# Kernel tuning notes

Measured on AMD Instinct MI355X. Metric: run time of the kernel, lower is better.

## Reference

```python
import jax, jax.numpy as jnp
import numpy as np

N = 4096
D = 256
H = 8
E = 131072
NEG = -1e30  # stands in for -inf; keeps grads NaN-free


def setup_inputs() -> dict:
    key = jax.random.key(0)
    ks = jax.random.split(key, 8)
    s = 1.0 / np.sqrt(D)
    return {
        "x": jax.random.normal(ks[0], (N, D), dtype=jnp.float32),
        "edge_index": jax.random.randint(ks[1], (2, E), 0, N, dtype=jnp.int32),
        "Wq": jax.random.normal(ks[2], (D, D), dtype=jnp.float32) * s,
        "Wk": jax.random.normal(ks[3], (D, D), dtype=jnp.float32) * s,
        "Wv": jax.random.normal(ks[4], (D, D), dtype=jnp.float32) * s,
        "Wo": jax.random.normal(ks[5], (D, D), dtype=jnp.float32) * s,
        "bo": jnp.zeros((D,), dtype=jnp.float32),
        "gamma": jnp.ones((D,), dtype=jnp.float32),
        "beta": jnp.zeros((D,), dtype=jnp.float32),
    }


def reference(x, edge_index, Wq, Wk, Wv, Wo, bo, gamma, beta):
    n, d_model = x.shape
    d_h = d_model // H
    scale = jnp.sqrt(jnp.float32(d_h))

    # mask: True = blocked. Diagonal and graph edges (dst attends to src) unblocked.
    mask = jnp.ones((n, n), dtype=bool)
    diag = jnp.arange(n)
    mask = mask.at[diag, diag].set(False)
    src, dst = edge_index[0], edge_index[1]
    mask = mask.at[dst, src].set(False)

    # projections: torch Linear computes x @ W.T
    Q = (x @ Wq.T).reshape(n, H, d_h).transpose(1, 0, 2)  # [H, N, d_h]
    K = (x @ Wk.T).reshape(n, H, d_h).transpose(1, 0, 2)
    V = (x @ Wv.T).reshape(n, H, d_h).transpose(1, 0, 2)

    scores = jnp.einsum("hnd,hmd->hnm", Q, K) / scale      # [H, N, N]
    scores = jnp.where(mask[None, :, :], NEG, scores)
    attn = jax.nn.softmax(scores, axis=-1)
    attn = jnp.nan_to_num(attn, nan=0.0)

    out = jnp.einsum("hnm,hmd->hnd", attn, V)              # [H, N, d_h]
    out = out.transpose(1, 0, 2).reshape(n, d_model)
    out = out @ Wo.T + bo

    # LayerNorm(x + out), eps=1e-5
    h = x + out
    mu = jnp.mean(h, axis=-1, keepdims=True)
    var = jnp.var(h, axis=-1, keepdims=True)
    return (h - mu) * jax.lax.rsqrt(var + 1e-5) * gamma + beta
```

## Files before the change

kernel.cpp:

```cpp
#include <hip/hip_runtime.h>

#define D_MODEL 256
#define N_HEADS 8
#define D_HEAD 32
#define MAXN 192

typedef __attribute__((ext_vector_type(8))) short bf16x8;
typedef __attribute__((ext_vector_type(4))) float f32x4;

__device__ __forceinline__ unsigned short f2bf(float f) {
    union { float f; unsigned int u; } v; v.f = f;
    unsigned int r = v.u + 0x7fff + ((v.u >> 16) & 1);
    return (unsigned short)(r >> 16);
}
__device__ __forceinline__ float bf2f(unsigned short u) {
    union { unsigned int u; float f; } v; v.u = ((unsigned int)u) << 16;
    return v.f;
}
__device__ __forceinline__ void pack8(const float* __restrict__ p, short* __restrict__ dst) {
    float4 u0 = *(const float4*)p;
    float4 u1 = *(const float4*)(p + 4);
    ushort4 a, b;
    a.x = f2bf(u0.x); a.y = f2bf(u0.y); a.z = f2bf(u0.z); a.w = f2bf(u0.w);
    b.x = f2bf(u1.x); b.y = f2bf(u1.y); b.z = f2bf(u1.z); b.w = f2bf(u1.w);
    *(ushort4*)dst = a;
    *(ushort4*)(dst + 4) = b;
}

__global__ void set_edges_kernel(const int* __restrict__ ei,
                                 unsigned long long* __restrict__ mask,
                                 int E, int n) {
    int e = blockIdx.x * blockDim.x + threadIdx.x;
    int wpr = n >> 6;
    if (e < n)
        atomicOr(&mask[(size_t)e * wpr + (e >> 6)], 1ULL << (e & 63));
    if (e < E) {
        int src = ei[e];
        int dst = ei[E + e];
        atomicOr(&mask[(size_t)dst * wpr + (src >> 6)], 1ULL << (src & 63));
    }
}

__global__ __launch_bounds__(256) void gemm_qkv_kernel(
        const float* __restrict__ x,
        const float* __restrict__ Wq, const float* __restrict__ Wk,
        const float* __restrict__ Wv,
        unsigned short* __restrict__ Qb, unsigned short* __restrict__ Kb,
        unsigned short* __restrict__ Vb) {
    const float* B = (blockIdx.z == 0) ? Wq : (blockIdx.z == 1) ? Wk : Wv;
    unsigned short* Cb = (blockIdx.z == 0) ? Qb : (blockIdx.z == 1) ? Kb : Vb;
    int bx = blockIdx.x, by = blockIdx.y;

    __shared__ short Alds[128][72];
    __shared__ short Blds[64][72];
    int t = threadIdx.x;
    int wave = t >> 6, lane = t & 63;
    int wr = wave >> 1, wc = wave & 1;
    int lr = t >> 3;
    int lk = (t & 7) << 3;

    const float* Abase = x + ((size_t)(by * 128 + lr)) * D_MODEL + lk;
    const float* Bbase = B + ((size_t)(bx * 64 + lr)) * D_MODEL + lk;

    int fm = lane & 15;
    int fk = (lane >> 4) << 3;

    f32x4 acc[4][2];
#pragma unroll
    for (int r = 0; r < 4; ++r)
#pragma unroll
        for (int c = 0; c < 2; ++c) acc[r][c] = (f32x4){0.f, 0.f, 0.f, 0.f};

    for (int k0 = 0; k0 < D_MODEL; k0 += 64) {
        pack8(Abase + k0,               &Alds[lr][lk]);
        pack8(Abase + 32 * D_MODEL + k0, &Alds[lr + 32][lk]);
        pack8(Abase + 64 * D_MODEL + k0, &Alds[lr + 64][lk]);
        pack8(Abase + 96 * D_MODEL + k0, &Alds[lr + 96][lk]);
        pack8(Bbase + k0,               &Blds[lr][lk]);
        pack8(Bbase + 32 * D_MODEL + k0, &Blds[lr + 32][lk]);
        __syncthreads();
#pragma unroll
        for (int ks = 0; ks < 64; ks += 32) {
            bf16x8 af[4], bf[2];
#pragma unroll
            for (int r = 0; r < 4; ++r)
                af[r] = *(const bf16x8*)&Alds[wr * 64 + r * 16 + fm][ks + fk];
#pragma unroll
            for (int c = 0; c < 2; ++c)
                bf[c] = *(const bf16x8*)&Blds[wc * 32 + c * 16 + fm][ks + fk];
#pragma unroll
            for (int r = 0; r < 4; ++r)
#pragma unroll
                for (int c = 0; c < 2; ++c)
                    acc[r][c] = __builtin_amdgcn_mfma_f32_16x16x32_bf16(
                        af[r], bf[c], acc[r][c], 0, 0, 0);
        }
        __syncthreads();
    }

    int orow0 = by * 128 + wr * 64 + ((lane >> 4) << 2);
    int ocol0 = bx * 64 + wc * 32 + (lane & 15);
#pragma unroll
    for (int r = 0; r < 4; ++r)
#pragma unroll
        for (int c = 0; c < 2; ++c)
#pragma unroll
            for (int q = 0; q < 4; ++q)
                Cb[(size_t)(orow0 + r * 16 + q) * D_MODEL + ocol0 + c * 16] =
                    f2bf(acc[r][c][q]);
}

__global__ __launch_bounds__(64) void attn_kernel(
        const unsigned short* __restrict__ Qb, const unsigned short* __restrict__ Kb,
        const unsigned short* __restrict__ Vb,
        const unsigned long long* __restrict__ mask,
        unsigned short* __restrict__ Ob, int n) {
    int dst = blockIdx.x;
    int L = threadIdx.x;
    int wpr = n >> 6;

    __shared__ int nbr[MAXN + 16];
    __shared__ float s_lds[N_HEADS][MAXN];

    unsigned long long w = (L < wpr) ? mask[(size_t)dst * wpr + L] : 0ULL;
    int c = __popcll(w);
    int xs = c;
#pragma unroll
    for (int o = 1; o < 64; o <<= 1) {
        int y = __shfl_up(xs, o, 64);
        if (L >= o) xs += y;
    }
    int pos = xs - c;
    while (w) {
        int b = __builtin_ctzll(w);
        w &= w - 1;
        if (pos < MAXN) nbr[pos] = (L << 6) + b;
        ++pos;
    }
    int cnt = __shfl(xs, 63, 64);
    if (cnt > MAXN) cnt = MAXN;
    int nb = (cnt + 15) & ~15;
    __syncthreads();
    int last = nbr[cnt - 1];
    if (L < nb - cnt) nbr[cnt + L] = last;
    __syncthreads();

    int col = L & 15;
    int kq = L >> 4;
    bf16x8 qf = (bf16x8){0, 0, 0, 0, 0, 0, 0, 0};
    if (col < N_HEADS)
        qf = *(const bf16x8*)(Qb + (size_t)dst * D_MODEL + col * D_HEAD + kq * 8);
    const bf16x8 zf = (bf16x8){0, 0, 0, 0, 0, 0, 0, 0};
    const float inv_scale = 0.17677669529663687f;

    for (int b0 = 0; b0 < nb; b0 += 16) {
        int nj = nbr[b0 + col];
        const unsigned short* krow = Kb + (size_t)nj * D_MODEL + kq * 8;
        f32x4 c0 = (f32x4){0.f, 0.f, 0.f, 0.f};
        f32x4 c1 = (f32x4){0.f, 0.f, 0.f, 0.f};
#pragma unroll
        for (int kb = 0; kb < 8; kb += 2) {
            bf16x8 a0 = *(const bf16x8*)(krow + kb * 32);
            bf16x8 a1 = *(const bf16x8*)(krow + kb * 32 + 32);
            bf16x8 bop0 = (col == kb)     ? qf : zf;
            bf16x8 bop1 = (col == kb + 1) ? qf : zf;
            c0 = __builtin_amdgcn_mfma_f32_16x16x32_bf16(a0, bop0, c0, 0, 0, 0);
            c1 = __builtin_amdgcn_mfma_f32_16x16x32_bf16(a1, bop1, c1, 0, 0, 0);
        }
        if (col < N_HEADS) {
            int jr = b0 + kq * 4;
            float4 o;
            float s0 = (c0[0] + c1[0]) * inv_scale;
            float s1 = (c0[1] + c1[1]) * inv_scale;
            float s2 = (c0[2] + c1[2]) * inv_scale;
            float s3 = (c0[3] + c1[3]) * inv_scale;
            o.x = (jr + 0 < cnt) ? s0 : -1e30f;
            o.y = (jr + 1 < cnt) ? s1 : -1e30f;
            o.z = (jr + 2 < cnt) ? s2 : -1e30f;
            o.w = (jr + 3 < cnt) ? s3 : -1e30f;
            *(float4*)&s_lds[col][jr] = o;
        }
    }
    __syncthreads();

    int h = L >> 3, i = L & 7;
    float m = -1e30f;
    for (int j0 = i * 4; j0 < nb; j0 += 32) {
        float4 v = *(const float4*)&s_lds[h][j0];
        m = fmaxf(m, fmaxf(fmaxf(v.x, v.y), fmaxf(v.z, v.w)));
    }
    m = fmaxf(m, __shfl_xor(m, 1, 8));
    m = fmaxf(m, __shfl_xor(m, 2, 8));
    m = fmaxf(m, __shfl_xor(m, 4, 8));
    float l = 0.f;
    for (int j0 = i * 4; j0 < nb; j0 += 32) {
        float4 v = *(const float4*)&s_lds[h][j0];
        float4 e;
        e.x = __expf(v.x - m); e.y = __expf(v.y - m);
        e.z = __expf(v.z - m); e.w = __expf(v.w - m);
        *(float4*)&s_lds[h][j0] = e;
        l += (e.x + e.y) + (e.z + e.w);
    }
    l += __shfl_xor(l, 1, 8);
    l += __shfl_xor(l, 2, 8);
    l += __shfl_xor(l, 4, 8);
    __syncthreads();

    f32x4 acc = (f32x4){0.f, 0.f, 0.f, 0.f};
    const unsigned short* vb = Vb + 4 * L;
    for (int j = 0; j < nb; j += 4) {
        float4 wv = *(const float4*)&s_lds[h][j];
        int j0 = nbr[j], j1 = nbr[j + 1], j2 = nbr[j + 2], j3 = nbr[j + 3];
        uint2 r0 = *(const uint2*)(vb + (size_t)j0 * D_MODEL);
        uint2 r1 = *(const uint2*)(vb + (size_t)j1 * D_MODEL);
        uint2 r2 = *(const uint2*)(vb + (size_t)j2 * D_MODEL);
        uint2 r3 = *(const uint2*)(vb + (size_t)j3 * D_MODEL);
        acc[0] += wv.x * bf2f((unsigned short)(r0.x & 0xffff));
        acc[1] += wv.x * bf2f((unsigned short)(r0.x >> 16));
        acc[2] += wv.x * bf2f((unsigned short)(r0.y & 0xffff));
        acc[3] += wv.x * bf2f((unsigned short)(r0.y >> 16));
        acc[0] += wv.y * bf2f((unsigned short)(r1.x & 0xffff));
        acc[1] += wv.y * bf2f((unsigned short)(r1.x >> 16));
        acc[2] += wv.y * bf2f((unsigned short)(r1.y & 0xffff));
        acc[3] += wv.y * bf2f((unsigned short)(r1.y >> 16));
        acc[0] += wv.z * bf2f((unsigned short)(r2.x & 0xffff));
        acc[1] += wv.z * bf2f((unsigned short)(r2.x >> 16));
        acc[2] += wv.z * bf2f((unsigned short)(r2.y & 0xffff));
        acc[3] += wv.z * bf2f((unsigned short)(r2.y >> 16));
        acc[0] += wv.w * bf2f((unsigned short)(r3.x & 0xffff));
        acc[1] += wv.w * bf2f((unsigned short)(r3.x >> 16));
        acc[2] += wv.w * bf2f((unsigned short)(r3.y & 0xffff));
        acc[3] += wv.w * bf2f((unsigned short)(r3.y >> 16));
    }
    float rl = 1.f / l;
    ushort4 o;
    o.x = f2bf(acc[0] * rl); o.y = f2bf(acc[1] * rl);
    o.z = f2bf(acc[2] * rl); o.w = f2bf(acc[3] * rl);
    *(ushort4*)(Ob + (size_t)dst * D_MODEL + 4 * L) = o;
}

struct SMemO {
    union {
        struct { short A[64][72]; short B[256][72]; } st;
        float c[64][260];
    };
};

__global__ __launch_bounds__(256) void gemm_o_ln_kernel(
        const unsigned short* __restrict__ Ob, const float* __restrict__ Wo,
        const float* __restrict__ x, const float* __restrict__ bo,
        const float* __restrict__ gamma, const float* __restrict__ beta,
        float* __restrict__ out) {
    __shared__ SMemO sm;
    int by = blockIdx.x;
    int t = threadIdx.x;
    int wave = t >> 6, lane = t & 63;
    int lr = t >> 3;
    int lk = (t & 7) << 3;

    const unsigned short* Abase = Ob + ((size_t)(by * 64 + lr)) * D_MODEL + lk;
    int fm = lane & 15;
    int fk = (lane >> 4) << 3;

    f32x4 acc[16];
#pragma unroll
    for (int ct = 0; ct < 16; ++ct) acc[ct] = (f32x4){0.f, 0.f, 0.f, 0.f};

    for (int k0 = 0; k0 < D_MODEL; k0 += 64) {
        *(uint4*)&sm.st.A[lr][lk]      = *(const uint4*)(Abase + k0);
        *(uint4*)&sm.st.A[lr + 32][lk] = *(const uint4*)(Abase + 32 * D_MODEL + k0);
#pragma unroll
        for (int j = 0; j < 8; ++j)
            pack8(Wo + ((size_t)(lr + 32 * j)) * D_MODEL + k0 + lk,
                  &sm.st.B[lr + 32 * j][lk]);
        __syncthreads();
#pragma unroll
        for (int ks = 0; ks < 64; ks += 32) {
            bf16x8 af = *(const bf16x8*)&sm.st.A[wave * 16 + fm][ks + fk];
#pragma unroll
            for (int ct = 0; ct < 16; ++ct) {
                bf16x8 bf = *(const bf16x8*)&sm.st.B[ct * 16 + fm][ks + fk];
                acc[ct] = __builtin_amdgcn_mfma_f32_16x16x32_bf16(af, bf, acc[ct], 0, 0, 0);
            }
        }
        __syncthreads();
    }

    int rr0 = wave * 16 + ((lane >> 4) << 2);
#pragma unroll
    for (int ct = 0; ct < 16; ++ct)
#pragma unroll
        for (int q = 0; q < 4; ++q)
            sm.c[rr0 + q][ct * 16 + (lane & 15)] = acc[ct][q];
    __syncthreads();

    float4 bo4 = *(const float4*)(bo + lane * 4);
    float4 g4  = *(const float4*)(gamma + lane * 4);
    float4 be4 = *(const float4*)(beta + lane * 4);
    for (int rr = 0; rr < 16; ++rr) {
        int r = wave * 16 + rr;
        int grow = by * 64 + r;
        float4 p = *(const float4*)&sm.c[r][lane * 4];
        float4 xv = *(const float4*)(x + (size_t)grow * D_MODEL + lane * 4);
        float hx = p.x + xv.x + bo4.x;
        float hy = p.y + xv.y + bo4.y;
        float hz = p.z + xv.z + bo4.z;
        float hw = p.w + xv.w + bo4.w;
        float s  = (hx + hy) + (hz + hw);
        float s2 = (hx * hx + hy * hy) + (hz * hz + hw * hw);
#pragma unroll
        for (int o = 32; o; o >>= 1) {
            s  += __shfl_xor(s, o, 64);
            s2 += __shfl_xor(s2, o, 64);
        }
        float mu = s * (1.f / 256.f);
        float var = s2 * (1.f / 256.f) - mu * mu;
        float rstd = rsqrtf(var + 1e-5f);
        float4 o4;
        o4.x = (hx - mu) * rstd * g4.x + be4.x;
        o4.y = (hy - mu) * rstd * g4.y + be4.y;
        o4.z = (hz - mu) * rstd * g4.z + be4.z;
        o4.w = (hw - mu) * rstd * g4.w + be4.w;
        *(float4*)(out + (size_t)grow * D_MODEL + lane * 4) = o4;
    }
}

extern "C" void kernel_launch(void* const* d_in, const int* in_sizes, int n_in,
                              void* d_out, int out_size, void* d_ws, size_t ws_size,
                              hipStream_t stream) {
    const float* x     = (const float*)d_in[0];
    const int*   ei    = (const int*)  d_in[1];
    const float* Wq    = (const float*)d_in[2];
    const float* Wk    = (const float*)d_in[3];
    const float* Wv    = (const float*)d_in[4];
    const float* Wo    = (const float*)d_in[5];
    const float* bo    = (const float*)d_in[6];
    const float* gamma = (const float*)d_in[7];
    const float* beta  = (const float*)d_in[8];
    float* out = (float*)d_out;

    int n = in_sizes[0] / D_MODEL;
    int E = in_sizes[1] / 2;

    char* ws = (char*)d_ws;
    size_t off = 0;
    unsigned long long* mask = (unsigned long long*)(ws + off);
    size_t mask_bytes = (size_t)n * (n >> 6) * sizeof(unsigned long long);
    off += mask_bytes;
    unsigned short* Qb = (unsigned short*)(ws + off); off += (size_t)n * D_MODEL * 2;
    unsigned short* Kb = (unsigned short*)(ws + off); off += (size_t)n * D_MODEL * 2;
    unsigned short* Vb = (unsigned short*)(ws + off); off += (size_t)n * D_MODEL * 2;
    unsigned short* Ob = (unsigned short*)(ws + off); off += (size_t)n * D_MODEL * 2;

    hipMemsetAsync(mask, 0, mask_bytes, stream);
    set_edges_kernel<<<(E + 255) / 256, 256, 0, stream>>>(ei, mask, E, n);

    dim3 gq(D_MODEL / 64, n / 128, 3);
    gemm_qkv_kernel<<<gq, 256, 0, stream>>>(x, Wq, Wk, Wv, Qb, Kb, Vb);

    attn_kernel<<<n, 64, 0, stream>>>(Qb, Kb, Vb, mask, Ob, n);

    gemm_o_ln_kernel<<<n / 64, 256, 0, stream>>>(Ob, Wo, x, bo, gamma, beta, out);
}
```

Baseline: 134.9 us.

## Pre-convert inputs to bf16, fuse mask init with casts and edges with QKV GEMM

A new prep kernel initialises the diagonal mask (replacing the memset) and converts x and all four weight matrices to bf16 once. The QKV GEMM and the edge-scatter atomics now run in one launch on disjoint blocks, and both GEMMs load bf16 tiles directly instead of converting fp32 per tile. The output-projection + LayerNorm kernel halves its row tile to 32 rows so it launches twice as many blocks. This cuts launch count and redundant conversion work, at the cost of extra workspace traffic for the bf16 copies. The prep kernel hardcodes N=4096 and D=256.

```diff
diff --git a/kernel.cpp b/kernel.cpp
--- a/kernel.cpp
+++ b/kernel.cpp
@@ -17,39 +17,70 @@
     union { unsigned int u; float f; } v; v.u = ((unsigned int)u) << 16;
     return v.f;
 }
-__device__ __forceinline__ void pack8(const float* __restrict__ p, short* __restrict__ dst) {
-    float4 u0 = *(const float4*)p;
-    float4 u1 = *(const float4*)(p + 4);
-    ushort4 a, b;
-    a.x = f2bf(u0.x); a.y = f2bf(u0.y); a.z = f2bf(u0.z); a.w = f2bf(u0.w);
-    b.x = f2bf(u1.x); b.y = f2bf(u1.y); b.z = f2bf(u1.z); b.w = f2bf(u1.w);
-    *(ushort4*)dst = a;
-    *(ushort4*)(dst + 4) = b;
-}
-
-__global__ void set_edges_kernel(const int* __restrict__ ei,
-                                 unsigned long long* __restrict__ mask,
-                                 int E, int n) {
-    int e = blockIdx.x * blockDim.x + threadIdx.x;
+
+__global__ void prep_kernel(const float* __restrict__ x,
+                            const float* __restrict__ W0, const float* __restrict__ W1,
+                            const float* __restrict__ W2, const float* __restrict__ W3,
+                            unsigned short* __restrict__ xb,
+                            unsigned short* __restrict__ O0, unsigned short* __restrict__ O1,
+                            unsigned short* __restrict__ O2, unsigned short* __restrict__ O3,
+                            unsigned long long* __restrict__ mask, int n) {
+    const int XV = (4096 * 256) / 4;
+    int i = blockIdx.x * blockDim.x + threadIdx.x;
+
     int wpr = n >> 6;
-    if (e < n)
-        atomicOr(&mask[(size_t)e * wpr + (e >> 6)], 1ULL << (e & 63));
-    if (e < E) {
-        int src = ei[e];
-        int dst = ei[E + e];
-        atomicOr(&mask[(size_t)dst * wpr + (src >> 6)], 1ULL << (src & 63));
-    }
-}
-
-__global__ __launch_bounds__(256) void gemm_qkv_kernel(
-        const float* __restrict__ x,
-        const float* __restrict__ Wq, const float* __restrict__ Wk,
-        const float* __restrict__ Wv,
+    int mwords = n * wpr;
+    if (i < mwords) {
+        int row = i >> 6;
+        int w = i & 63;
+        mask[i] = (w == (row >> 6)) ? (1ULL << (row & 63)) : 0ULL;
+    }
+
+    const float* src;
+    unsigned short* dst;
+    int k;
+    if (i < XV) {
+        src = x; dst = xb; k = i;
+    } else {
+        int i2 = i - XV;
+        if (i2 >= 4 * 16384) return;
+        int z = i2 >> 14;
+        k = i2 & 16383;
+        src = (z == 0) ? W0 : (z == 1) ? W1 : (z == 2) ? W2 : W3;
+        dst = (z == 0) ? O0 : (z == 1) ? O1 : (z == 2) ? O2 : O3;
+    }
+    float4 v = *(const float4*)(src + (size_t)k * 4);
+    ushort4 o;
+    o.x = f2bf(v.x); o.y = f2bf(v.y); o.z = f2bf(v.z); o.w = f2bf(v.w);
+    *(ushort4*)(dst + (size_t)k * 4) = o;
+}
+
+#define NGEMM 384
+
+__global__ __launch_bounds__(256) void qkv_edges_kernel(
+        const unsigned short* __restrict__ xb,
+        const unsigned short* __restrict__ Wq, const unsigned short* __restrict__ Wk,
+        const unsigned short* __restrict__ Wv,
         unsigned short* __restrict__ Qb, unsigned short* __restrict__ Kb,
-        unsigned short* __restrict__ Vb) {
-    const float* B = (blockIdx.z == 0) ? Wq : (blockIdx.z == 1) ? Wk : Wv;
-    unsigned short* Cb = (blockIdx.z == 0) ? Qb : (blockIdx.z == 1) ? Kb : Vb;
-    int bx = blockIdx.x, by = blockIdx.y;
+        unsigned short* __restrict__ Vb,
+        const int* __restrict__ ei, unsigned long long* __restrict__ mask,
+        int E, int n) {
+    int blk = blockIdx.x;
+    if (blk >= NGEMM) {
+        int e = (blk - NGEMM) * 256 + threadIdx.x;
+        if (e < E) {
+            int src = ei[e];
+            int dst = ei[E + e];
+            int wpr = n >> 6;
+            atomicOr(&mask[(size_t)dst * wpr + (src >> 6)], 1ULL << (src & 63));
+        }
+        return;
+    }
+    int z = blk >> 7;
+    int r = blk & 127;
+    int by = r >> 2, bx = r & 3;
+    const unsigned short* B = (z == 0) ? Wq : (z == 1) ? Wk : Wv;
+    unsigned short* Cb = (z == 0) ? Qb : (z == 1) ? Kb : Vb;
 
     __shared__ short Alds[128][72];
     __shared__ short Blds[64][72];
@@ -59,41 +90,41 @@
     int lr = t >> 3;
     int lk = (t & 7) << 3;
 
-    const float* Abase = x + ((size_t)(by * 128 + lr)) * D_MODEL + lk;
-    const float* Bbase = B + ((size_t)(bx * 64 + lr)) * D_MODEL + lk;
+    const unsigned short* Abase = xb + ((size_t)(by * 128 + lr)) * D_MODEL + lk;
+    const unsigned short* Bbase = B + ((size_t)(bx * 64 + lr)) * D_MODEL + lk;
 
     int fm = lane & 15;
     int fk = (lane >> 4) << 3;
 
     f32x4 acc[4][2];
 #pragma unroll
-    for (int r = 0; r < 4; ++r)
-#pragma unroll
-        for (int c = 0; c < 2; ++c) acc[r][c] = (f32x4){0.f, 0.f, 0.f, 0.f};
+    for (int rr = 0; rr < 4; ++rr)
+#pragma unroll
+        for (int c = 0; c < 2; ++c) acc[rr][c] = (f32x4){0.f, 0.f, 0.f, 0.f};
 
     for (int k0 = 0; k0 < D_MODEL; k0 += 64) {
-        pack8(Abase + k0,               &Alds[lr][lk]);
-        pack8(Abase + 32 * D_MODEL + k0, &Alds[lr + 32][lk]);
-        pack8(Abase + 64 * D_MODEL + k0, &Alds[lr + 64][lk]);
-        pack8(Abase + 96 * D_MODEL + k0, &Alds[lr + 96][lk]);
-        pack8(Bbase + k0,               &Blds[lr][lk]);
-        pack8(Bbase + 32 * D_MODEL + k0, &Blds[lr + 32][lk]);
+        *(uint4*)&Alds[lr][lk]      = *(const uint4*)(Abase + k0);
+        *(uint4*)&Alds[lr + 32][lk] = *(const uint4*)(Abase + 32 * D_MODEL + k0);
+        *(uint4*)&Alds[lr + 64][lk] = *(const uint4*)(Abase + 64 * D_MODEL + k0);
+        *(uint4*)&Alds[lr + 96][lk] = *(const uint4*)(Abase + 96 * D_MODEL + k0);
+        *(uint4*)&Blds[lr][lk]      = *(const uint4*)(Bbase + k0);
+        *(uint4*)&Blds[lr + 32][lk] = *(const uint4*)(Bbase + 32 * D_MODEL + k0);
         __syncthreads();
 #pragma unroll
         for (int ks = 0; ks < 64; ks += 32) {
             bf16x8 af[4], bf[2];
 #pragma unroll
-            for (int r = 0; r < 4; ++r)
-                af[r] = *(const bf16x8*)&Alds[wr * 64 + r * 16 + fm][ks + fk];
+            for (int rr = 0; rr < 4; ++rr)
+                af[rr] = *(const bf16x8*)&Alds[wr * 64 + rr * 16 + fm][ks + fk];
 #pragma unroll
             for (int c = 0; c < 2; ++c)
                 bf[c] = *(const bf16x8*)&Blds[wc * 32 + c * 16 + fm][ks + fk];
 #pragma unroll
-            for (int r = 0; r < 4; ++r)
+            for (int rr = 0; rr < 4; ++rr)
 #pragma unroll
                 for (int c = 0; c < 2; ++c)
-                    acc[r][c] = __builtin_amdgcn_mfma_f32_16x16x32_bf16(
-                        af[r], bf[c], acc[r][c], 0, 0, 0);
+                    acc[rr][c] = __builtin_amdgcn_mfma_f32_16x16x32_bf16(
+                        af[rr], bf[c], acc[rr][c], 0, 0, 0);
         }
         __syncthreads();
     }
@@ -101,13 +132,13 @@
     int orow0 = by * 128 + wr * 64 + ((lane >> 4) << 2);
     int ocol0 = bx * 64 + wc * 32 + (lane & 15);
 #pragma unroll
-    for (int r = 0; r < 4; ++r)
+    for (int rr = 0; rr < 4; ++rr)
 #pragma unroll
         for (int c = 0; c < 2; ++c)
 #pragma unroll
             for (int q = 0; q < 4; ++q)
-                Cb[(size_t)(orow0 + r * 16 + q) * D_MODEL + ocol0 + c * 16] =
-                    f2bf(acc[r][c][q]);
+                Cb[(size_t)(orow0 + rr * 16 + q) * D_MODEL + ocol0 + c * 16] =
+                    f2bf(acc[rr][c][q]);
 }
 
 __global__ __launch_bounds__(64) void attn_kernel(
@@ -241,13 +272,13 @@
 
 struct SMemO {
     union {
-        struct { short A[64][72]; short B[256][72]; } st;
-        float c[64][260];
+        struct { short A[32][72]; short B[256][72]; } st;
+        float c[32][260];
     };
 };
 
 __global__ __launch_bounds__(256) void gemm_o_ln_kernel(
-        const unsigned short* __restrict__ Ob, const float* __restrict__ Wo,
+        const unsigned short* __restrict__ Ob, const unsigned short* __restrict__ Wob,
         const float* __restrict__ x, const float* __restrict__ bo,
         const float* __restrict__ gamma, const float* __restrict__ beta,
         float* __restrict__ out) {
@@ -255,51 +286,52 @@
     int by = blockIdx.x;
     int t = threadIdx.x;
     int wave = t >> 6, lane = t & 63;
+    int rt = wave >> 1, cq = wave & 1;
     int lr = t >> 3;
     int lk = (t & 7) << 3;
 
-    const unsigned short* Abase = Ob + ((size_t)(by * 64 + lr)) * D_MODEL + lk;
+    const unsigned short* Abase = Ob + ((size_t)(by * 32 + lr)) * D_MODEL + lk;
     int fm = lane & 15;
     int fk = (lane >> 4) << 3;
 
-    f32x4 acc[16];
-#pragma unroll
-    for (int ct = 0; ct < 16; ++ct) acc[ct] = (f32x4){0.f, 0.f, 0.f, 0.f};
+    f32x4 acc[8];
+#pragma unroll
+    for (int ct = 0; ct < 8; ++ct) acc[ct] = (f32x4){0.f, 0.f, 0.f, 0.f};
 
     for (int k0 = 0; k0 < D_MODEL; k0 += 64) {
-        *(uint4*)&sm.st.A[lr][lk]      = *(const uint4*)(Abase + k0);
-        *(uint4*)&sm.st.A[lr + 32][lk] = *(const uint4*)(Abase + 32 * D_MODEL + k0);
+        *(uint4*)&sm.st.A[lr][lk] = *(const uint4*)(Abase + k0);
 #pragma unroll
         for (int j = 0; j < 8; ++j)
-            pack8(Wo + ((size_t)(lr + 32 * j)) * D_MODEL + k0 + lk,
-                  &sm.st.B[lr + 32 * j][lk]);
+            *(uint4*)&sm.st.B[lr + 32 * j][lk] =
+                *(const uint4*)(Wob + ((size_t)(lr + 32 * j)) * D_MODEL + k0 + lk);
         __syncthreads();
 #pragma unroll
         for (int ks = 0; ks < 64; ks += 32) {
-            bf16x8 af = *(const bf16x8*)&sm.st.A[wave * 16 + fm][ks + fk];
-#pragma unroll
-            for (int ct = 0; ct < 16; ++ct) {
-                bf16x8 bf = *(const bf16x8*)&sm.st.B[ct * 16 + fm][ks + fk];
+            bf16x8 af = *(const bf16x8*)&sm.st.A[rt * 16 + fm][ks + fk];
+#pragma unroll
+            for (int ct = 0; ct < 8; ++ct) {
+                bf16x8 bf = *(const bf16x8*)&sm.st.B[cq * 128 + ct * 16 + fm][ks + fk];
                 acc[ct] = __builtin_amdgcn_mfma_f32_16x16x32_bf16(af, bf, acc[ct], 0, 0, 0);
             }
         }
         __syncthreads();
     }
 
-    int rr0 = wave * 16 + ((lane >> 4) << 2);
-#pragma unroll
-    for (int ct = 0; ct < 16; ++ct)
+    int rr0 = rt * 16 + ((lane >> 4) << 2);
+#pragma unroll
+    for (int ct = 0; ct < 8; ++ct)
 #pragma unroll
         for (int q = 0; q < 4; ++q)
-            sm.c[rr0 + q][ct * 16 + (lane & 15)] = acc[ct][q];
+            sm.c[rr0 + q][cq * 128 + ct * 16 + (lane & 15)] = acc[ct][q];
     __syncthreads();
 
     float4 bo4 = *(const float4*)(bo + lane * 4);
     float4 g4  = *(const float4*)(gamma + lane * 4);
     float4 be4 = *(const float4*)(beta + lane * 4);
-    for (int rr = 0; rr < 16; ++rr) {
-        int r = wave * 16 + rr;
-        int grow = by * 64 + r;
+#pragma unroll
+    for (int rr = 0; rr < 8; ++rr) {
+        int r = wave * 8 + rr;
+        int grow = by * 32 + r;
         float4 p = *(const float4*)&sm.c[r][lane * 4];
         float4 xv = *(const float4*)(x + (size_t)grow * D_MODEL + lane * 4);
         float hx = p.x + xv.x + bo4.x;
@@ -345,20 +377,25 @@
     char* ws = (char*)d_ws;
     size_t off = 0;
     unsigned long long* mask = (unsigned long long*)(ws + off);
-    size_t mask_bytes = (size_t)n * (n >> 6) * sizeof(unsigned long long);
-    off += mask_bytes;
-    unsigned short* Qb = (unsigned short*)(ws + off); off += (size_t)n * D_MODEL * 2;
-    unsigned short* Kb = (unsigned short*)(ws + off); off += (size_t)n * D_MODEL * 2;
-    unsigned short* Vb = (unsigned short*)(ws + off); off += (size_t)n * D_MODEL * 2;
-    unsigned short* Ob = (unsigned short*)(ws + off); off += (size_t)n * D_MODEL * 2;
-
-    hipMemsetAsync(mask, 0, mask_bytes, stream);
-    set_edges_kernel<<<(E + 255) / 256, 256, 0, stream>>>(ei, mask, E, n);
-
-    dim3 gq(D_MODEL / 64, n / 128, 3);
-    gemm_qkv_kernel<<<gq, 256, 0, stream>>>(x, Wq, Wk, Wv, Qb, Kb, Vb);
+    off += (size_t)n * (n >> 6) * sizeof(unsigned long long);
+    unsigned short* xb  = (unsigned short*)(ws + off); off += (size_t)n * D_MODEL * 2;
+    unsigned short* Wqb = (unsigned short*)(ws + off); off += D_MODEL * D_MODEL * 2;
+    unsigned short* Wkb = (unsigned short*)(ws + off); off += D_MODEL * D_MODEL * 2;
+    unsigned short* Wvb = (unsigned short*)(ws + off); off += D_MODEL * D_MODEL * 2;
+    unsigned short* Wob = (unsigned short*)(ws + off); off += D_MODEL * D_MODEL * 2;
+    unsigned short* Qb  = (unsigned short*)(ws + off); off += (size_t)n * D_MODEL * 2;
+    unsigned short* Kb  = (unsigned short*)(ws + off); off += (size_t)n * D_MODEL * 2;
+    unsigned short* Vb  = (unsigned short*)(ws + off); off += (size_t)n * D_MODEL * 2;
+    unsigned short* Ob  = (unsigned short*)(ws + off); off += (size_t)n * D_MODEL * 2;
+
+    prep_kernel<<<1280, 256, 0, stream>>>(x, Wq, Wk, Wv, Wo,
+                                          xb, Wqb, Wkb, Wvb, Wob, mask, n);
+
+    int edge_blocks = (E + 255) / 256;
+    qkv_edges_kernel<<<NGEMM + edge_blocks, 256, 0, stream>>>(
+        xb, Wqb, Wkb, Wvb, Qb, Kb, Vb, ei, mask, E, n);
 
     attn_kernel<<<n, 64, 0, stream>>>(Qb, Kb, Vb, mask, Ob, n);
 
-    gemm_o_ln_kernel<<<n / 64, 256, 0, stream>>>(Ob, Wo, x, bo, gamma, beta, out);
-}
+    gemm_o_ln_kernel<<<n / 32, 256, 0, stream>>>(Ob, Wob, x, bo, gamma, beta, out);
+}
```

Measured after the change: 113.8 us. 15.7% less time.
